# Optimization experiments

Measured on AMD Instinct MI355X. Metric: run time of the kernel, lower is better.

The kernel has to match this reference:

```python
import jax, jax.numpy as jnp
import numpy as np

DIM = 1024
HEADS = 16
HEAD_DIM = DIM // HEADS
SCALE = HEAD_DIM ** -0.5
HIDDEN = 4 * DIM
EPS = 1e-5


def _ln(x, g, b):
    m = jnp.mean(x, -1, keepdims=True)
    v = jnp.mean(jnp.square(x - m), -1, keepdims=True)
    return (x - m) / jnp.sqrt(v + EPS) * g + b


def _attn(x, wqkv, qb, vb, wp, bp):
    # x: (B, N, C). qkv bias = concat(q_bias, zeros, v_bias) as in the torch code.
    B, N, C = x.shape
    bias = jnp.concatenate([qb, jnp.zeros_like(vb), vb])
    qkv = (x @ wqkv.T + bias).reshape(B, N, 3, HEADS, HEAD_DIM).transpose(2, 0, 3, 1, 4)
    q, k, v = qkv[0], qkv[1], qkv[2]
    # qk_float=True: logits computed in float32
    logits = jnp.einsum('bhqd,bhkd->bhqk', (q * SCALE).astype(jnp.float32), k.astype(jnp.float32))
    a = jax.nn.softmax(logits, axis=-1).astype(x.dtype)
    o = jnp.einsum('bhqk,bhkd->bqhd', a, v).reshape(B, N, C)
    return o @ wp.T + bp


def setup_inputs() -> dict:
    key = jax.random.key(0)
    ks = jax.random.split(key, 16)
    s = 0.02
    d = {
        'x': jax.random.normal(ks[0], (4, 8, 196, DIM), jnp.float32),
        'cls_token': jax.random.normal(ks[1], (4, DIM), jnp.float32),
        # temporal branch
        'tln_g': jnp.ones((DIM,), jnp.float32), 'tln_b': jnp.zeros((DIM,), jnp.float32),
        't_wqkv': jax.random.normal(ks[2], (3 * DIM, DIM), jnp.float32) * s,
        't_qb': jax.random.normal(ks[3], (DIM,), jnp.float32) * s,
        't_vb': jax.random.normal(ks[4], (DIM,), jnp.float32) * s,
        't_wproj': jax.random.normal(ks[5], (DIM, DIM), jnp.float32) * s,
        't_bproj': jnp.zeros((DIM,), jnp.float32),
        't_fc_w': jax.random.normal(ks[6], (DIM, DIM), jnp.float32) * s,
        't_fc_b': jnp.zeros((DIM,), jnp.float32),
        # spatial branch
        'n1_g': jnp.ones((DIM,), jnp.float32), 'n1_b': jnp.zeros((DIM,), jnp.float32),
        's_wqkv': jax.random.normal(ks[7], (3 * DIM, DIM), jnp.float32) * s,
        's_qb': jax.random.normal(ks[8], (DIM,), jnp.float32) * s,
        's_vb': jax.random.normal(ks[9], (DIM,), jnp.float32) * s,
        's_wproj': jax.random.normal(ks[10], (DIM, DIM), jnp.float32) * s,
        's_bproj': jnp.zeros((DIM,), jnp.float32),
        # mlp
        'n2_g': jnp.ones((DIM,), jnp.float32), 'n2_b': jnp.zeros((DIM,), jnp.float32),
        'fc1_w': jax.random.normal(ks[11], (HIDDEN, DIM), jnp.float32) * s,
        'fc1_b': jnp.zeros((HIDDEN,), jnp.float32),
        'fc2_w': jax.random.normal(ks[12], (DIM, HIDDEN), jnp.float32) * s,
        'fc2_b': jnp.zeros((DIM,), jnp.float32),
    }
    return d


def reference(x, cls_token, tln_g, tln_b, t_wqkv, t_qb, t_vb, t_wproj, t_bproj,
              t_fc_w, t_fc_b, n1_g, n1_b, s_wqkv, s_qb, s_vb, s_wproj, s_bproj,
              n2_g, n2_b, fc1_w, fc1_b, fc2_w, fc2_b):
    B, T, N, C = x.shape
    # temporal attention: 'b t n m -> (b n) t m'
    xt = x.transpose(0, 2, 1, 3).reshape(B * N, T, C)
    xt = _attn(_ln(xt, tln_g, tln_b), t_wqkv, t_qb, t_vb, t_wproj, t_bproj)
    # '(b n) t m -> b (n t) m'
    xt = xt.reshape(B, N * T, C)
    xt = xt @ t_fc_w.T + t_fc_b
    xt = x.transpose(0, 2, 1, 3).reshape(B, N * T, C) + xt
    # spatial attention with cls token per frame
    init_cls = cls_token[:, None, :]                               # (B, 1, C)
    cls_rep = jnp.broadcast_to(init_cls, (B, T, C)).reshape(B * T, 1, C)
    xs = xt.reshape(B, N, T, C).transpose(0, 2, 1, 3).reshape(B * T, N, C)
    xs = jnp.concatenate([cls_rep, xs], axis=1)                    # (B*T, N+1, C)
    xs = _attn(_ln(xs, n1_g, n1_b), s_wqkv, s_qb, s_vb, s_wproj, s_bproj)
    cls_m = xs[:, 0, :].reshape(B, T, C).mean(axis=1, keepdims=True)  # (B, 1, C)
    xs = xs[:, 1:, :].reshape(B, T, N, C).transpose(0, 2, 1, 3).reshape(B, N * T, C)
    x2 = jnp.concatenate([init_cls, xt], axis=1) + jnp.concatenate([cls_m, xs], axis=1)
    # MLP (exact GELU, matching nn.GELU default)
    h = _ln(x2, n2_g, n2_b)
    h = jax.nn.gelu(h @ fc1_w.T + fc1_b, approximate=False) @ fc2_w.T + fc2_b
    x2 = x2 + h
    cls_out = x2[:, 0, :]
    xo = x2[:, 1:].reshape(B, N, T, C).transpose(0, 2, 1, 3)       # (B, T, N, C)
    return xo, cls_out
```

## Files before the change

kernel.cpp:

```cpp
#include <hip/hip_runtime.h>
#include <stdint.h>


#define SCALE 0.125f

typedef unsigned short u16;
typedef short bf16x8 __attribute__((ext_vector_type(8)));
typedef float f32x4 __attribute__((ext_vector_type(4)));

static constexpr int kNT    = 1568;
static constexpr int kRowsA = 6272;
static constexpr int kSeqS  = 197;
static constexpr int kRowsS = 6304;
static constexpr int kRowsC = 6276;
static constexpr size_t kXO = 6422528;

__device__ __forceinline__ float bf2f(u16 u) {
    union { unsigned int i; float f; } c; c.i = ((unsigned int)u) << 16; return c.f;
}
__device__ __forceinline__ u16 f2bf(float f) {
    union { float f; unsigned int i; } c; c.f = f;
    unsigned int r = c.i + 0x7FFFu + ((c.i >> 16) & 1u);
    return (u16)(r >> 16);
}

__device__ __forceinline__ void gll16(const void* g, void* l) {
    __builtin_amdgcn_global_load_lds((__attribute__((address_space(1))) void*)g,
                                     (__attribute__((address_space(3))) void*)l,
                                     16, 0, 0);
}

__global__ void convw_k(const float* __restrict__ in, u16* __restrict__ out, int n4) {
    const int stride = gridDim.x * blockDim.x;
    for (int i = blockIdx.x * blockDim.x + threadIdx.x; i < n4; i += stride) {
        float4 v = ((const float4*)in)[i];
        ushort4 o;
        o.x = f2bf(v.x); o.y = f2bf(v.y); o.z = f2bf(v.z); o.w = f2bf(v.w);
        ((ushort4*)out)[i] = o;
    }
}

__global__ void bias3_k(const float* __restrict__ qb, const float* __restrict__ vb,
                        float* __restrict__ dst) {
    const int i = blockIdx.x * 256 + threadIdx.x;
    if (i >= 3072) return;
    dst[i] = (i < 1024) ? qb[i] : (i < 2048) ? 0.0f : vb[i - 2048];
}

template<int MODE>
__global__ void ln_k(const float* __restrict__ src, const float* __restrict__ src2,
                     const float* __restrict__ g, const float* __restrict__ bt,
                     u16* __restrict__ out, int rows) {
    const int r = (blockIdx.x << 2) + (threadIdx.x >> 6);
    const int lane = threadIdx.x & 63;
    if (r >= rows) return;
    const float* srow;
    if constexpr (MODE == 0) {
        int b = r / kNT, rem = r - b * kNT, n = rem >> 3, t = rem & 7;
        srow = src + (((size_t)((b * 8 + t) * 196 + n)) << 10);
    } else if constexpr (MODE == 1) {
        int s2 = r / kSeqS, i = r - s2 * kSeqS, b = s2 >> 3, t = s2 & 7;
        srow = (i == 0) ? (src2 + ((size_t)b << 10))
                        : (src + (((size_t)(b * kNT + ((i - 1) << 3) + t)) << 10));
    } else {
        srow = src + ((size_t)r << 10);
    }
    float4 v[4]; float s = 0.f, ss = 0.f;
#pragma unroll
    for (int j = 0; j < 4; ++j) {
        v[j] = *(const float4*)&srow[((j << 6) + lane) << 2];
        s  += v[j].x + v[j].y + v[j].z + v[j].w;
        ss += v[j].x * v[j].x + v[j].y * v[j].y + v[j].z * v[j].z + v[j].w * v[j].w;
    }
#pragma unroll
    for (int off = 1; off < 64; off <<= 1) { s += __shfl_xor(s, off); ss += __shfl_xor(ss, off); }
    const float mean = s * (1.f / 1024.f);
    const float rstd = rsqrtf(ss * (1.f / 1024.f) - mean * mean + 1e-5f);
#pragma unroll
    for (int j = 0; j < 4; ++j) {
        const int c = ((j << 6) + lane) << 2;
        float4 gg = *(const float4*)&g[c];
        float4 bb = *(const float4*)&bt[c];
        ushort4 o;
        o.x = f2bf((v[j].x - mean) * rstd * gg.x + bb.x);
        o.y = f2bf((v[j].y - mean) * rstd * gg.y + bb.y);
        o.z = f2bf((v[j].z - mean) * rstd * gg.z + bb.z);
        o.w = f2bf((v[j].w - mean) * rstd * gg.w + bb.w);
        *(ushort4*)&out[((size_t)r << 10) + c] = o;
    }
}

template<int MODE, int TM>
__global__ __launch_bounds__(256, 4) void gemm_bt(
        const u16* __restrict__ A, const u16* __restrict__ W,
        const float* __restrict__ bias,
        u16* __restrict__ outB, float* __restrict__ outF,
        const float* __restrict__ resid, float* __restrict__ dout,
        int M, int N, int K) {
    constexpr int MF  = TM / 32;
    constexpr int NCA = TM / 64;
    __shared__ __align__(16) u16 As[2][TM * 32];
    __shared__ __align__(16) u16 Bs[2][128 * 32];
    const int tid  = threadIdx.x;
    const int lane = tid & 63, wave = tid >> 6;
    const int lo = lane & 15, hi = lane >> 4;
    const int wr = wave >> 1, wc = wave & 1;
    const int row0 = blockIdx.y * TM, col0 = blockIdx.x << 7;

    const u16* aP[NCA]; const u16* bP[2];
#pragma unroll
    for (int i = 0; i < NCA; ++i) {
        const int c = wave * TM + (i << 6) + lane;
        const int row = c >> 2;
        const int jl = (((c & 3) ^ (row & 3)) << 3);
        int ar = row0 + row; if (ar > M - 1) ar = M - 1;
        aP[i] = A + (size_t)ar * K + jl;
    }
#pragma unroll
    for (int i = 0; i < 2; ++i) {
        const int c = (wave << 7) + (i << 6) + lane;
        const int row = c >> 2;
        const int jl = (((c & 3) ^ (row & 3)) << 3);
        int br = col0 + row; if (br > N - 1) br = N - 1;
        bP[i] = W + (size_t)br * K + jl;
    }

    f32x4 acc[MF][4] = {};
    const int nk = K >> 5;

    auto stage = [&](int buf, int k0) {
#pragma unroll
        for (int i = 0; i < NCA; ++i)
            gll16(aP[i] + k0, &As[buf][wave * (TM * 8) + (i << 9)]);
#pragma unroll
        for (int i = 0; i < 2; ++i)
            gll16(bP[i] + k0, &Bs[buf][(wave << 10) + (i << 9)]);
    };

    stage(0, 0);
    __syncthreads();

    int cur = 0;
    for (int it = 0; it < nk; ++it) {
        const bool more = (it + 1) < nk;
        if (more) stage(cur ^ 1, (it + 1) << 5);
        const int sl = (hi ^ (lo & 3)) << 3;
        bf16x8 af[MF], bfr[4];
#pragma unroll
        for (int m = 0; m < MF; ++m)
            af[m] = *(const bf16x8*)&As[cur][((wr * (TM / 2) + (m << 4) + lo) << 5) + sl];
#pragma unroll
        for (int n = 0; n < 4; ++n)
            bfr[n] = *(const bf16x8*)&Bs[cur][(((wc << 6) + (n << 4) + lo) << 5) + sl];
#pragma unroll
        for (int m = 0; m < MF; ++m)
#pragma unroll
            for (int n = 0; n < 4; ++n)
                acc[m][n] = __builtin_amdgcn_mfma_f32_16x16x32_bf16(af[m], bfr[n], acc[m][n], 0, 0, 0);
        if (more) {
            __syncthreads();
            cur ^= 1;
        }
    }

#pragma unroll
    for (int m = 0; m < MF; ++m) {
        const int rb = row0 + wr * (TM / 2) + (m << 4) + (hi << 2);
#pragma unroll
        for (int n = 0; n < 4; ++n) {
            const int c = col0 + (wc << 6) + (n << 4) + lo;
            const float bc = bias[c];
#pragma unroll
            for (int j = 0; j < 4; ++j) {
                const int r = rb + j;
                if (r >= M) continue;
                float v = acc[m][n][j] + bc;
                if constexpr (MODE == 2) v = 0.5f * v * (1.0f + erff(v * 0.70710678f));
                if constexpr (MODE == 3) {
                    int b = r / 1568, rem = r - b * 1568, nn = rem >> 3, tt = rem & 7;
                    v += resid[(((size_t)((b * 8 + tt) * 196 + nn)) << 10) + c];
                }
                if constexpr (MODE == 0 || MODE == 2) {
                    outB[(size_t)r * N + c] = f2bf(v);
                } else if constexpr (MODE == 1 || MODE == 3) {
                    outF[(size_t)r * N + c] = v;
                } else {
                    v += resid[((size_t)r << 10) + c];
                    int b = r / 1569, i = r - b * 1569;
                    if (i == 0) dout[kXO + ((size_t)b << 10) + c] = v;
                    else {
                        int jj = i - 1, nn = jj >> 3, tt = jj & 7;
                        dout[(((size_t)((b * 8 + tt) * 196 + nn)) << 10) + c] = v;
                    }
                }
            }
        }
    }
}

__global__ void attn_a_k(const u16* __restrict__ qkv, u16* __restrict__ o) {
    __shared__ float lq[4][8][65], lk[4][8][65], lv[4][8][65];
    __shared__ float al[4][64];
    const int lane = threadIdx.x & 63, wave = threadIdx.x >> 6;
    const int p = (blockIdx.x << 2) + wave;
    const int s = p >> 4, h = p & 15;
    const u16* base = qkv + (size_t)s * 24576 + (h << 6);
    for (int u = lane; u < 1536; u += 64) {
        const int part = u >> 9, t = (u >> 6) & 7, d = u & 63;
        const float val = bf2f(base[(size_t)t * 3072 + (part << 10) + d]);
        if (part == 0) lq[wave][t][d] = val;
        else if (part == 1) lk[wave][t][d] = val;
        else lv[wave][t][d] = val;
    }
    __syncthreads();
    const int qi = lane >> 3, kj = lane & 7;
    float dot = 0.f;
#pragma unroll
    for (int d = 0; d < 64; ++d) dot += lq[wave][qi][d] * lk[wave][kj][d];
    dot *= SCALE;
    float m = dot;
    m = fmaxf(m, __shfl_xor(m, 1));
    m = fmaxf(m, __shfl_xor(m, 2));
    m = fmaxf(m, __shfl_xor(m, 4));
    const float e = expf(dot - m);
    float sm = e;
    sm += __shfl_xor(sm, 1);
    sm += __shfl_xor(sm, 2);
    sm += __shfl_xor(sm, 4);
    al[wave][lane] = e / sm;
    __syncthreads();
    u16* orow = o + (size_t)s * 8192 + (h << 6) + lane;
#pragma unroll
    for (int ii = 0; ii < 8; ++ii) {
        float accv = 0.f;
#pragma unroll
        for (int jj = 0; jj < 8; ++jj) accv += al[wave][(ii << 3) + jj] * lv[wave][jj][lane];
        orow[(size_t)ii * 1024] = f2bf(accv);
    }
}

__global__ __launch_bounds__(256, 2) void attn_s_mfma(const u16* __restrict__ qkv,
                                                      u16* __restrict__ o) {
    __shared__ __align__(16) u16 SM[29696];
    u16* __restrict__ Vt = SM;
    const int tid = threadIdx.x, lane = tid & 63, wave = tid >> 6;
    const int lo = lane & 15, hi = lane >> 4;
    u16* __restrict__ Pw = SM + 14848 + wave * 3712;
    const int s2 = blockIdx.x >> 4, h = blockIdx.x & 15;
    const u16* __restrict__ base = qkv + (size_t)s2 * (kSeqS * 3072) + (h << 6);

    for (int u = tid; u < 26 * 64; u += 256) {
        const int d = u & 63, k0 = (u >> 6) << 3;
        union { bf16x8 v; u16 e[8]; } pk;
#pragma unroll
        for (int i = 0; i < 8; ++i) {
            int kr = k0 + i; if (kr > 196) kr = 196;
            pk.e[i] = base[(size_t)kr * 3072 + 2048 + d];
        }
        *(bf16x8*)&Vt[d * 232 + k0] = pk.v;
    }
    for (int u = tid; u < 1024; u += 256)
        Vt[(u >> 4) * 232 + 208 + (u & 15)] = 0;
    for (int u = lane; u < 256; u += 64)
        Pw[(u >> 4) * 232 + 208 + (u & 15)] = 0;
    __syncthreads();

    for (int qt = wave; qt < 13; qt += 4) {
        int qr = qt * 16 + lo; if (qr > 196) qr = 196;
        const u16* qp = base + (size_t)qr * 3072;
        const bf16x8 aq0 = *(const bf16x8*)&qp[hi << 3];
        const bf16x8 aq1 = *(const bf16x8*)&qp[32 + (hi << 3)];

        f32x4 s[13];
#pragma unroll
        for (int kt = 0; kt < 13; ++kt) {
            int kr = kt * 16 + lo; if (kr > 196) kr = 196;
            const u16* kp = base + (size_t)kr * 3072 + 1024;
            const bf16x8 bk0 = *(const bf16x8*)&kp[hi << 3];
            const bf16x8 bk1 = *(const bf16x8*)&kp[32 + (hi << 3)];
            f32x4 acc = {};
            acc = __builtin_amdgcn_mfma_f32_16x16x32_bf16(aq0, bk0, acc, 0, 0, 0);
            acc = __builtin_amdgcn_mfma_f32_16x16x32_bf16(aq1, bk1, acc, 0, 0, 0);
            s[kt] = acc * SCALE;
        }
        if (lo > 4) s[12] = (f32x4){-1e30f, -1e30f, -1e30f, -1e30f};

        float inv[4];
#pragma unroll
        for (int j = 0; j < 4; ++j) {
            float m = s[0][j];
#pragma unroll
            for (int kt = 1; kt < 13; ++kt) m = fmaxf(m, s[kt][j]);
            m = fmaxf(m, __shfl_xor(m, 1));
            m = fmaxf(m, __shfl_xor(m, 2));
            m = fmaxf(m, __shfl_xor(m, 4));
            m = fmaxf(m, __shfl_xor(m, 8));
            float sum = 0.f;
#pragma unroll
            for (int kt = 0; kt < 13; ++kt) {
                const float e = __expf(s[kt][j] - m);
                s[kt][j] = e;
                sum += e;
            }
            sum += __shfl_xor(sum, 1);
            sum += __shfl_xor(sum, 2);
            sum += __shfl_xor(sum, 4);
            sum += __shfl_xor(sum, 8);
            inv[j] = 1.f / sum;
        }

#pragma unroll
        for (int kt = 0; kt < 13; ++kt)
#pragma unroll
            for (int j = 0; j < 4; ++j)
                Pw[((hi << 2) + j) * 232 + kt * 16 + lo] = f2bf(s[kt][j]);

        f32x4 o4[4] = {};
#pragma unroll
        for (int kc = 0; kc < 7; ++kc) {
            const bf16x8 pa = *(const bf16x8*)&Pw[lo * 232 + kc * 32 + (hi << 3)];
#pragma unroll
            for (int dt = 0; dt < 4; ++dt) {
                const bf16x8 vf = *(const bf16x8*)&Vt[(dt * 16 + lo) * 232 + kc * 32 + (hi << 3)];
                o4[dt] = __builtin_amdgcn_mfma_f32_16x16x32_bf16(pa, vf, o4[dt], 0, 0, 0);
            }
        }

#pragma unroll
        for (int j = 0; j < 4; ++j) {
            const int q = qt * 16 + (hi << 2) + j;
            if (q > 196) continue;
            u16* orow = o + (((size_t)(s2 * kSeqS + q)) << 10) + (h << 6);
#pragma unroll
            for (int dt = 0; dt < 4; ++dt)
                orow[dt * 16 + lo] = f2bf(o4[dt][j] * inv[j]);
        }
    }
}

__global__ void clsm_k(const float* __restrict__ xs, float* __restrict__ cm) {
    const int idx = blockIdx.x * 256 + threadIdx.x;
    if (idx >= 4096) return;
    const int b = idx >> 10, c = idx & 1023;
    float s = 0.f;
#pragma unroll
    for (int t = 0; t < 8; ++t) s += xs[(((size_t)(b * 8 + t)) * kSeqS) * 1024 + c];
    cm[idx] = s * 0.125f;
}

__global__ void build_x2_k(const float* __restrict__ xt, const float* __restrict__ xs,
                           const float* __restrict__ cls, const float* __restrict__ cm,
                           float* __restrict__ x2) {
    const int r = blockIdx.x;
    const int c = threadIdx.x << 2;
    const int b = r / 1569, i = r - b * 1569;
    const float* pa; const float* pb;
    if (i == 0) {
        pa = cls + ((size_t)b << 10) + c;
        pb = cm + ((size_t)b << 10) + c;
    } else {
        const int jj = i - 1, n = jj >> 3, t = jj & 7;
        pa = xt + (((size_t)(b * 1568 + jj)) << 10) + c;
        pb = xs + (((size_t)((b * 8 + t) * kSeqS + 1 + n)) << 10) + c;
    }
    const float4 va = *(const float4*)pa;
    const float4 vb = *(const float4*)pb;
    float4 vo;
    vo.x = va.x + vb.x; vo.y = va.y + vb.y; vo.z = va.z + vb.z; vo.w = va.w + vb.w;
    *(float4*)&x2[((size_t)r << 10) + c] = vo;
}

extern "C" void kernel_launch(void* const* d_in, const int* in_sizes, int n_in,
                              void* d_out, int out_size, void* d_ws, size_t ws_size,
                              hipStream_t stream) {
    const float* x       = (const float*)d_in[0];
    const float* cls     = (const float*)d_in[1];
    const float* tln_g   = (const float*)d_in[2];
    const float* tln_b   = (const float*)d_in[3];
    const float* t_wqkv  = (const float*)d_in[4];
    const float* t_qb    = (const float*)d_in[5];
    const float* t_vb    = (const float*)d_in[6];
    const float* t_wproj = (const float*)d_in[7];
    const float* t_bproj = (const float*)d_in[8];
    const float* t_fc_w  = (const float*)d_in[9];
    const float* t_fc_b  = (const float*)d_in[10];
    const float* n1_g    = (const float*)d_in[11];
    const float* n1_b    = (const float*)d_in[12];
    const float* s_wqkv  = (const float*)d_in[13];
    const float* s_qb    = (const float*)d_in[14];
    const float* s_vb    = (const float*)d_in[15];
    const float* s_wproj = (const float*)d_in[16];
    const float* s_bproj = (const float*)d_in[17];
    const float* n2_g    = (const float*)d_in[18];
    const float* n2_b    = (const float*)d_in[19];
    const float* fc1_w   = (const float*)d_in[20];
    const float* fc1_b   = (const float*)d_in[21];
    const float* fc2_w   = (const float*)d_in[22];
    const float* fc2_b   = (const float*)d_in[23];
    float* dout = (float*)d_out;
    char* ws = (char*)d_ws;

    size_t off = 0;
    auto alloc = [&](size_t bytes) { size_t o = off; off += (bytes + 255) & ~(size_t)255; return o; };

    u16* t_wqkv_bf  = (u16*)(ws + alloc(3145728ull * 2));
    u16* t_wproj_bf = (u16*)(ws + alloc(1048576ull * 2));
    u16* t_fcw_bf   = (u16*)(ws + alloc(1048576ull * 2));
    u16* s_wqkv_bf  = (u16*)(ws + alloc(3145728ull * 2));
    u16* s_wproj_bf = (u16*)(ws + alloc(1048576ull * 2));
    u16* fc1_bf     = (u16*)(ws + alloc(4194304ull * 2));
    u16* fc2_bf     = (u16*)(ws + alloc(4194304ull * 2));
    u16* ln_bf      = (u16*)(ws + alloc((size_t)kRowsS * 1024 * 2));
    u16* qkv_bf     = (u16*)(ws + alloc((size_t)kRowsS * 3072 * 2));
    u16* o_bf       = (u16*)(ws + alloc((size_t)kRowsS * 1024 * 2));
    u16* h1_bf      = qkv_bf;
    u16* mid_bf     = (u16*)(ws + alloc((size_t)kRowsA * 1024 * 2));
    float* xt_f     = (float*)(ws + alloc((size_t)kRowsA * 1024 * 4));
    float* xs_f     = (float*)(ws + alloc((size_t)kRowsS * 1024 * 4));
    float* x2_f     = (float*)(ws + alloc((size_t)kRowsC * 1024 * 4));
    float* bias_t   = (float*)(ws + alloc(3072 * 4));
    float* bias_s   = (float*)(ws + alloc(3072 * 4));
    float* clsm     = (float*)(ws + alloc(4096 * 4));
    (void)ws_size; (void)in_sizes; (void)n_in; (void)out_size;

    convw_k<<<dim3(1024), dim3(256), 0, stream>>>(t_wqkv, t_wqkv_bf, 786432);
    convw_k<<<dim3(512),  dim3(256), 0, stream>>>(t_wproj, t_wproj_bf, 262144);
    convw_k<<<dim3(512),  dim3(256), 0, stream>>>(t_fc_w, t_fcw_bf, 262144);
    convw_k<<<dim3(1024), dim3(256), 0, stream>>>(s_wqkv, s_wqkv_bf, 786432);
    convw_k<<<dim3(512),  dim3(256), 0, stream>>>(s_wproj, s_wproj_bf, 262144);
    convw_k<<<dim3(1024), dim3(256), 0, stream>>>(fc1_w, fc1_bf, 1048576);
    convw_k<<<dim3(1024), dim3(256), 0, stream>>>(fc2_w, fc2_bf, 1048576);
    bias3_k<<<dim3(12), dim3(256), 0, stream>>>(t_qb, t_vb, bias_t);
    bias3_k<<<dim3(12), dim3(256), 0, stream>>>(s_qb, s_vb, bias_s);

    ln_k<0><<<dim3(kRowsA / 4), dim3(256), 0, stream>>>(x, nullptr, tln_g, tln_b, ln_bf, kRowsA);
    gemm_bt<0, 128><<<dim3(24, 49), dim3(256), 0, stream>>>(ln_bf, t_wqkv_bf, bias_t, qkv_bf, nullptr, nullptr, nullptr, kRowsA, 3072, 1024);
    attn_a_k<<<dim3(3136), dim3(256), 0, stream>>>(qkv_bf, o_bf);
    gemm_bt<0, 64><<<dim3(8, 98), dim3(256), 0, stream>>>(o_bf, t_wproj_bf, t_bproj, mid_bf, nullptr, nullptr, nullptr, kRowsA, 1024, 1024);
    gemm_bt<3, 64><<<dim3(8, 98), dim3(256), 0, stream>>>(mid_bf, t_fcw_bf, t_fc_b, nullptr, xt_f, x, nullptr, kRowsA, 1024, 1024);

    ln_k<1><<<dim3(kRowsS / 4), dim3(256), 0, stream>>>(xt_f, cls, n1_g, n1_b, ln_bf, kRowsS);
    gemm_bt<0, 128><<<dim3(24, 50), dim3(256), 0, stream>>>(ln_bf, s_wqkv_bf, bias_s, qkv_bf, nullptr, nullptr, nullptr, kRowsS, 3072, 1024);
    attn_s_mfma<<<dim3(512), dim3(256), 0, stream>>>(qkv_bf, o_bf);
    gemm_bt<1, 64><<<dim3(8, 99), dim3(256), 0, stream>>>(o_bf, s_wproj_bf, s_bproj, nullptr, xs_f, nullptr, nullptr, kRowsS, 1024, 1024);
    clsm_k<<<dim3(16), dim3(256), 0, stream>>>(xs_f, clsm);
    build_x2_k<<<dim3(kRowsC), dim3(256), 0, stream>>>(xt_f, xs_f, cls, clsm, x2_f);

    ln_k<2><<<dim3(kRowsC / 4), dim3(256), 0, stream>>>(x2_f, nullptr, n2_g, n2_b, ln_bf, kRowsC);
    gemm_bt<2, 128><<<dim3(32, 50), dim3(256), 0, stream>>>(ln_bf, fc1_bf, fc1_b, h1_bf, nullptr, nullptr, nullptr, kRowsC, 4096, 1024);
    gemm_bt<4, 64><<<dim3(8, 99), dim3(256), 0, stream>>>(h1_bf, fc2_bf, fc2_b, nullptr, nullptr, x2_f, dout, kRowsC, 1024, 4096);
}
```

Measured before the change: 553.8 us.

## Triple-buffer GEMM LDS staging with vmcnt waits and single barrier per step

Moves the bf16 GEMM main loop from double to triple buffering of the LDS tiles. Two K-tiles are prefetched, and each iteration waits with explicit s_waitcnt vmcnt on the older loads, then issues one barrier before staging the tile two steps ahead. The LDS XOR swizzle is also changed, with matching write and read index formulas, to reduce bank conflicts. The extra LDS buffer lowers the occupancy hint to 3 blocks for larger tiles, and correctness relies on the hand-counted vmcnt values.

Measured after the change: 582.6 us. 1.05x slower.

```diff
diff --git a/kernel.cpp b/kernel.cpp
--- a/kernel.cpp
+++ b/kernel.cpp
@@ -91,7 +91,7 @@
 }
 
 template<int MODE, int TM>
-__global__ __launch_bounds__(256, 4) void gemm_bt(
+__global__ __launch_bounds__(256, (TM == 64 ? 4 : 3)) void gemm_bt(
         const u16* __restrict__ A, const u16* __restrict__ W,
         const float* __restrict__ bias,
         u16* __restrict__ outB, float* __restrict__ outF,
@@ -99,8 +99,9 @@
         int M, int N, int K) {
     constexpr int MF  = TM / 32;
     constexpr int NCA = TM / 64;
-    __shared__ __align__(16) u16 As[2][TM * 32];
-    __shared__ __align__(16) u16 Bs[2][128 * 32];
+    constexpr int LPT = NCA + 2;
+    __shared__ __align__(16) u16 As[3][TM * 32];
+    __shared__ __align__(16) u16 Bs[3][128 * 32];
     const int tid  = threadIdx.x;
     const int lane = tid & 63, wave = tid >> 6;
     const int lo = lane & 15, hi = lane >> 4;
@@ -112,7 +113,7 @@
     for (int i = 0; i < NCA; ++i) {
         const int c = wave * TM + (i << 6) + lane;
         const int row = c >> 2;
-        const int jl = (((c & 3) ^ (row & 3)) << 3);
+        const int jl = (((c & 3) ^ ((c >> 3) & 3)) << 3);
         int ar = row0 + row; if (ar > M - 1) ar = M - 1;
         aP[i] = A + (size_t)ar * K + jl;
     }
@@ -120,7 +121,7 @@
     for (int i = 0; i < 2; ++i) {
         const int c = (wave << 7) + (i << 6) + lane;
         const int row = c >> 2;
-        const int jl = (((c & 3) ^ (row & 3)) << 3);
+        const int jl = (((c & 3) ^ ((c >> 3) & 3)) << 3);
         int br = col0 + row; if (br > N - 1) br = N - 1;
         bP[i] = W + (size_t)br * K + jl;
     }
@@ -128,7 +129,8 @@
     f32x4 acc[MF][4] = {};
     const int nk = K >> 5;
 
-    auto stage = [&](int buf, int k0) {
+    auto stage = [&](int buf, int kt) {
+        const int k0 = kt << 5;
 #pragma unroll
         for (int i = 0; i < NCA; ++i)
             gll16(aP[i] + k0, &As[buf][wave * (TM * 8) + (i << 9)]);
@@ -138,29 +140,37 @@
     };
 
     stage(0, 0);
-    __syncthreads();
-
-    int cur = 0;
-    for (int it = 0; it < nk; ++it) {
-        const bool more = (it + 1) < nk;
-        if (more) stage(cur ^ 1, (it + 1) << 5);
-        const int sl = (hi ^ (lo & 3)) << 3;
+    stage(1, 1);
+
+    const int sl = (hi ^ ((lo >> 1) & 3)) << 3;
+    int bc = 0;
+    for (int t = 0; t < nk; ++t) {
+        if (t + 1 < nk) {
+            if constexpr (LPT == 3) asm volatile("s_waitcnt vmcnt(3)" ::: "memory");
+            else                    asm volatile("s_waitcnt vmcnt(4)" ::: "memory");
+        } else {
+            asm volatile("s_waitcnt vmcnt(0)" ::: "memory");
+        }
+        __builtin_amdgcn_s_barrier();
+        __builtin_amdgcn_sched_barrier(0);
+        asm volatile("" ::: "memory");
+        if (t + 2 < nk) {
+            int bs = bc + 2; if (bs >= 3) bs -= 3;
+            stage(bs, t + 2);
+        }
         bf16x8 af[MF], bfr[4];
 #pragma unroll
         for (int m = 0; m < MF; ++m)
-            af[m] = *(const bf16x8*)&As[cur][((wr * (TM / 2) + (m << 4) + lo) << 5) + sl];
+            af[m] = *(const bf16x8*)&As[bc][((wr * (TM / 2) + (m << 4) + lo) << 5) + sl];
 #pragma unroll
         for (int n = 0; n < 4; ++n)
-            bfr[n] = *(const bf16x8*)&Bs[cur][(((wc << 6) + (n << 4) + lo) << 5) + sl];
+            bfr[n] = *(const bf16x8*)&Bs[bc][(((wc << 6) + (n << 4) + lo) << 5) + sl];
 #pragma unroll
         for (int m = 0; m < MF; ++m)
 #pragma unroll
             for (int n = 0; n < 4; ++n)
                 acc[m][n] = __builtin_amdgcn_mfma_f32_16x16x32_bf16(af[m], bfr[n], acc[m][n], 0, 0, 0);
-        if (more) {
-            __syncthreads();
-            cur ^= 1;
-        }
+        if (++bc == 3) bc = 0;
     }
 
 #pragma unroll
@@ -169,12 +179,12 @@
 #pragma unroll
         for (int n = 0; n < 4; ++n) {
             const int c = col0 + (wc << 6) + (n << 4) + lo;
-            const float bc = bias[c];
+            const float bc2 = bias[c];
 #pragma unroll
             for (int j = 0; j < 4; ++j) {
                 const int r = rb + j;
                 if (r >= M) continue;
-                float v = acc[m][n][j] + bc;
+                float v = acc[m][n][j] + bc2;
                 if constexpr (MODE == 2) v = 0.5f * v * (1.0f + erff(v * 0.70710678f));
                 if constexpr (MODE == 3) {
                     int b = r / 1568, rem = r - b * 1568, nn = rem >> 3, tt = rem & 7;
```
